# Kernel optimization log

Hardware: AMD Instinct MI355X
Metric: run time of the kernel (lower is better)

The kernel has to match this reference:

```python
import jax, jax.numpy as jnp
import numpy as np

N_NODES = 100000


def gcn_conv(x, W, b, src, dst, n):
    """PyG GCNConv with default add_self_loops and symmetric normalization."""
    xw = x @ W  # [N, out]
    loop = jnp.arange(n, dtype=src.dtype)
    s = jnp.concatenate([src, loop])  # source j
    d = jnp.concatenate([dst, loop])  # target i
    deg = jax.ops.segment_sum(jnp.ones_like(d, dtype=xw.dtype), d, num_segments=n)
    dinv = jnp.where(deg > 0, jax.lax.rsqrt(deg), 0.0)
    norm = dinv[s] * dinv[d]  # [E+N]
    msg = xw[s] * norm[:, None]
    out = jax.ops.segment_sum(msg, d, num_segments=n)
    return out + b


def setup_inputs() -> dict:
    key = jax.random.key(0)
    ks = jax.random.split(key, 9)
    n, e, f = N_NODES, 1600000, 512
    x = jax.random.normal(ks[0], (n, f), dtype=jnp.float32)
    edge_index = jax.random.randint(ks[1], (2, e), 0, n, dtype=jnp.int32)
    y = jax.random.uniform(ks[2], (n, 1), dtype=jnp.float32)
    W1 = jax.random.normal(ks[3], (f, 64), dtype=jnp.float32) / np.sqrt(f)
    b1 = jnp.zeros((64,), jnp.float32)
    W2 = jax.random.normal(ks[4], (64, 256), dtype=jnp.float32) / np.sqrt(64)
    b2 = jnp.zeros((256,), jnp.float32)
    W3 = jax.random.normal(ks[5], (256, 1), dtype=jnp.float32) / np.sqrt(256)
    b3 = jnp.zeros((1,), jnp.float32)
    return {"x": x, "edge_index": edge_index, "y": y,
            "W1": W1, "b1": b1, "W2": W2, "b2": b2, "W3": W3, "b3": b3}


def reference(x, edge_index, y, W1, b1, W2, b2, W3, b3):
    n = x.shape[0]
    src, dst = edge_index[0], edge_index[1]
    h = jax.nn.relu(gcn_conv(x, W1, b1, src, dst, n))
    # dropout is identity in eval mode
    h = jax.nn.relu(gcn_conv(h, W2, b2, src, dst, n))
    z = gcn_conv(h, W3, b3, src, dst, n)  # logits [N, 1]
    # BCE(sigmoid(z), y), computed stably via log-sigmoid
    loss = -(y * jax.nn.log_sigmoid(z) + (1.0 - y) * jax.nn.log_sigmoid(-z))
    return jnp.mean(loss)
```

## Files before the change

kernel.cpp:

```cpp
#include <hip/hip_runtime.h>
#include <math.h>

typedef __attribute__((ext_vector_type(8))) short s16x8;
typedef __attribute__((ext_vector_type(4))) float f32x4;

__device__ inline ushort f2bf(float f) {
    union { float f; unsigned u; } v; v.f = f;
    unsigned r = v.u + 0x7FFF + ((v.u >> 16) & 1);
    return (ushort)(r >> 16);
}
__device__ inline float bf2f(ushort h) {
    union { unsigned u; float f; } v; v.u = ((unsigned)h) << 16;
    return v.f;
}
__device__ inline float bfLo(unsigned u) {
    union { unsigned x; float f; } v; v.x = u << 16; return v.f;
}
__device__ inline float bfHi(unsigned u) {
    union { unsigned x; float f; } v; v.x = u & 0xFFFF0000u; return v.f;
}


__global__ void hist_kernel(const int* __restrict__ dst, int E, int* __restrict__ cnt) {
    int e = blockIdx.x * blockDim.x + threadIdx.x;
    if (e < E) atomicAdd(&cnt[dst[e]], 1);
}

__global__ void alloc_kernel(const int* __restrict__ cnt, int* __restrict__ row_start,
                             float* __restrict__ dinv, int* __restrict__ total, int N) {
    int i = blockIdx.x * blockDim.x + threadIdx.x;
    int lane = threadIdx.x & 63;
    int c = (i < N) ? cnt[i] : 0;
    int inc = c;
#pragma unroll
    for (int o = 1; o < 64; o <<= 1) {
        int v = __shfl_up(inc, o, 64);
        if (lane >= o) inc += v;
    }
    int wsum = __shfl(inc, 63, 64);
    int base = 0;
    if (lane == 0) base = atomicAdd(total, wsum);
    base = __shfl(base, 0, 64);
    if (i < N) {
        row_start[i] = base + inc - c;
        dinv[i] = rsqrtf((float)(c + 1));
    }
}

__global__ void scatter_kernel(const int* __restrict__ src, const int* __restrict__ dst, int E,
                               const int* __restrict__ row_start, int* __restrict__ cursor,
                               int* __restrict__ csr) {
    int e = blockIdx.x * blockDim.x + threadIdx.x;
    if (e < E) {
        int d = dst[e];
        int p = row_start[d] + atomicAdd(&cursor[d], 1);
        csr[p] = src[e];
    }
}

__global__ void wsplit_kernel(const float* __restrict__ W, ushort* __restrict__ wt_hi,
                              ushort* __restrict__ wt_lo) {
    int idx = blockIdx.x * blockDim.x + threadIdx.x;
    if (idx < 64 * 512) {
        int n = idx & 63, k = idx >> 6;
        float f = W[k * 64 + n];
        ushort h = f2bf(f);
        wt_hi[n * 512 + k] = h;
        wt_lo[n * 512 + k] = f2bf(f - bf2f(h));
    }
}

__global__ __launch_bounds__(256, 3) void gemm1_kernel(const float* __restrict__ x,
                                                       const ushort* __restrict__ wt_hi,
                                                       const ushort* __restrict__ wt_lo,
                                                       const float* __restrict__ dinv,
                                                       ushort* __restrict__ out, int N) {
    __shared__ __align__(16) short xs_hi[128 * 64];
    __shared__ __align__(16) short xs_lo[128 * 64];
    __shared__ __align__(16) short ws_hi[64 * 64];
    __shared__ __align__(16) short ws_lo[64 * 64];

    const int tid = threadIdx.x;
    const int nodeBase = blockIdx.x * 128;
    const int wave = tid >> 6, lane = tid & 63;
    const int m16 = lane & 15, quad = lane >> 4;

    f32x4 acc[2][4];
#pragma unroll
    for (int mt = 0; mt < 2; mt++)
#pragma unroll
        for (int nt = 0; nt < 4; nt++) acc[mt][nt] = (f32x4){0.f, 0.f, 0.f, 0.f};

    for (int kc = 0; kc < 512; kc += 64) {
        __syncthreads();
#pragma unroll
        for (int i = 0; i < 4; i++) {
            int f = tid + i * 256;
            int node = f >> 3, g = f & 7;
            int gn = nodeBase + node;
            if (gn >= N) gn = N - 1;
            const float4 a = *(const float4*)(x + (size_t)gn * 512 + kc + g * 8);
            const float4 b = *(const float4*)(x + (size_t)gn * 512 + kc + g * 8 + 4);
            float ff[8] = {a.x, a.y, a.z, a.w, b.x, b.y, b.z, b.w};
            union { ushort u[8]; uint4 v; } H, L;
#pragma unroll
            for (int j = 0; j < 8; j++) {
                ushort h = f2bf(ff[j]);
                H.u[j] = h;
                L.u[j] = f2bf(ff[j] - bf2f(h));
            }
            int gp = (g + node) & 7;
            *(uint4*)&xs_hi[node * 64 + gp * 8] = H.v;
            *(uint4*)&xs_lo[node * 64 + gp * 8] = L.v;
        }
#pragma unroll
        for (int i = 0; i < 2; i++) {
            int f = tid + i * 256;
            int n = f >> 3, g = f & 7;
            int gp = (g + n) & 7;
            *(uint4*)&ws_hi[n * 64 + gp * 8] =
                *(const uint4*)(wt_hi + (size_t)n * 512 + kc + g * 8);
            *(uint4*)&ws_lo[n * 64 + gp * 8] =
                *(const uint4*)(wt_lo + (size_t)n * 512 + kc + g * 8);
        }
        __syncthreads();
#pragma unroll
        for (int ck = 0; ck < 2; ck++) {
            s16x8 Ah[2], Al[2];
#pragma unroll
            for (int mt = 0; mt < 2; mt++) {
                int row = (wave * 2 + mt) * 16 + m16;
                int gp = (ck * 4 + quad + row) & 7;
                Ah[mt] = *(s16x8*)&xs_hi[row * 64 + gp * 8];
                Al[mt] = *(s16x8*)&xs_lo[row * 64 + gp * 8];
            }
#pragma unroll
            for (int nt = 0; nt < 4; nt++) {
                int n = nt * 16 + m16;
                int gp = (ck * 4 + quad + n) & 7;
                s16x8 Bh = *(s16x8*)&ws_hi[n * 64 + gp * 8];
                s16x8 Bl = *(s16x8*)&ws_lo[n * 64 + gp * 8];
#pragma unroll
                for (int mt = 0; mt < 2; mt++) {
                    acc[mt][nt] = __builtin_amdgcn_mfma_f32_16x16x32_bf16(Ah[mt], Bh, acc[mt][nt], 0, 0, 0);
                    acc[mt][nt] = __builtin_amdgcn_mfma_f32_16x16x32_bf16(Ah[mt], Bl, acc[mt][nt], 0, 0, 0);
                    acc[mt][nt] = __builtin_amdgcn_mfma_f32_16x16x32_bf16(Al[mt], Bh, acc[mt][nt], 0, 0, 0);
                }
            }
        }
    }
#pragma unroll
    for (int mt = 0; mt < 2; mt++) {
#pragma unroll
        for (int r = 0; r < 4; r++) {
            int gn = nodeBase + (wave * 2 + mt) * 16 + quad * 4 + r;
            if (gn < N) {
                float di = dinv[gn];
#pragma unroll
                for (int nt = 0; nt < 4; nt++)
                    out[(size_t)gn * 64 + nt * 16 + m16] = f2bf(di * acc[mt][nt][r]);
            }
        }
    }
}

template <int RELU, int BIAS, int PREMUL>
__global__ void agg64bf_kernel(const ushort* __restrict__ in, ushort* __restrict__ out,
                               const int* __restrict__ row_start, const int* __restrict__ cnt,
                               const int* __restrict__ csr, const float* __restrict__ dinv,
                               const float* __restrict__ bias, int N) {
    int gw = (int)((blockIdx.x * (size_t)blockDim.x + threadIdx.x) >> 6);
    int lane = threadIdx.x & 63;
    if (gw >= N) return;
    float acc = bf2f(in[(size_t)gw * 64 + lane]);
    int s = row_start[gw];
    int c = cnt[gw];
    int e = 0;
    for (; e + 8 <= c; e += 8) {
        int j0 = csr[s + e + 0], j1 = csr[s + e + 1], j2 = csr[s + e + 2], j3 = csr[s + e + 3];
        int j4 = csr[s + e + 4], j5 = csr[s + e + 5], j6 = csr[s + e + 6], j7 = csr[s + e + 7];
        float v0 = bf2f(in[(size_t)j0 * 64 + lane]);
        float v1 = bf2f(in[(size_t)j1 * 64 + lane]);
        float v2 = bf2f(in[(size_t)j2 * 64 + lane]);
        float v3 = bf2f(in[(size_t)j3 * 64 + lane]);
        float v4 = bf2f(in[(size_t)j4 * 64 + lane]);
        float v5 = bf2f(in[(size_t)j5 * 64 + lane]);
        float v6 = bf2f(in[(size_t)j6 * 64 + lane]);
        float v7 = bf2f(in[(size_t)j7 * 64 + lane]);
        acc += ((v0 + v1) + (v2 + v3)) + ((v4 + v5) + (v6 + v7));
    }
    for (; e < c; e++) {
        int j = csr[s + e];
        acc += bf2f(in[(size_t)j * 64 + lane]);
    }
    float di = dinv[gw];
    float v = di * acc;
    if (BIAS) v += bias[lane];
    if (RELU) v = fmaxf(v, 0.f);
    if (PREMUL) v *= di;
    out[(size_t)gw * 64 + lane] = f2bf(v);
}

__global__ __launch_bounds__(256, 2) void gemm23_kernel(const ushort* __restrict__ a2,
                                                        const float* __restrict__ W2,
                                                        const float* __restrict__ b2,
                                                        const float* __restrict__ W3,
                                                        const float* __restrict__ dinv,
                                                        float* __restrict__ r, int N) {
    __shared__ float w2s[64 * 256];
    __shared__ float b2s[256];
    __shared__ float w3s[256];
    const int tid = threadIdx.x;
#pragma unroll
    for (int i = 0; i < 16; i++) {
        int f4 = tid + i * 256;
        *(float4*)&w2s[f4 * 4] = *(const float4*)&W2[f4 * 4];
    }
    b2s[tid] = b2[tid];
    w3s[tid] = W3[tid];
    __syncthreads();

    const int lane = tid & 63;
    const int wave = tid >> 6;
    const int nodeBase = blockIdx.x * 64 + wave * 16;

    float4 w3f = *(const float4*)&w3s[lane * 4];
    float4 b2f = *(const float4*)&b2s[lane * 4];

    float acc[16][4];
#pragma unroll
    for (int n = 0; n < 16; n++) {
        acc[n][0] = 0.f; acc[n][1] = 0.f; acc[n][2] = 0.f; acc[n][3] = 0.f;
    }

    for (int k4 = 0; k4 < 64; k4 += 4) {
        float4 wf0 = *(const float4*)&w2s[(k4 + 0) * 256 + lane * 4];
        float4 wf1 = *(const float4*)&w2s[(k4 + 1) * 256 + lane * 4];
        float4 wf2 = *(const float4*)&w2s[(k4 + 2) * 256 + lane * 4];
        float4 wf3 = *(const float4*)&w2s[(k4 + 3) * 256 + lane * 4];
#pragma unroll
        for (int n = 0; n < 16; n++) {
            int gn = nodeBase + n;
            if (gn >= N) gn = N - 1;
            uint2 u = *(const uint2*)(a2 + (size_t)gn * 64 + k4);
            float a0 = bfLo(u.x), a1 = bfHi(u.x), a2v = bfLo(u.y), a3 = bfHi(u.y);
            acc[n][0] = fmaf(a0, wf0.x, acc[n][0]);
            acc[n][1] = fmaf(a0, wf0.y, acc[n][1]);
            acc[n][2] = fmaf(a0, wf0.z, acc[n][2]);
            acc[n][3] = fmaf(a0, wf0.w, acc[n][3]);
            acc[n][0] = fmaf(a1, wf1.x, acc[n][0]);
            acc[n][1] = fmaf(a1, wf1.y, acc[n][1]);
            acc[n][2] = fmaf(a1, wf1.z, acc[n][2]);
            acc[n][3] = fmaf(a1, wf1.w, acc[n][3]);
            acc[n][0] = fmaf(a2v, wf2.x, acc[n][0]);
            acc[n][1] = fmaf(a2v, wf2.y, acc[n][1]);
            acc[n][2] = fmaf(a2v, wf2.z, acc[n][2]);
            acc[n][3] = fmaf(a2v, wf2.w, acc[n][3]);
            acc[n][0] = fmaf(a3, wf3.x, acc[n][0]);
            acc[n][1] = fmaf(a3, wf3.y, acc[n][1]);
            acc[n][2] = fmaf(a3, wf3.z, acc[n][2]);
            acc[n][3] = fmaf(a3, wf3.w, acc[n][3]);
        }
    }

#pragma unroll
    for (int n = 0; n < 16; n++) {
        float r0 = fmaxf(acc[n][0] + b2f.x, 0.f);
        float r1 = fmaxf(acc[n][1] + b2f.y, 0.f);
        float r2 = fmaxf(acc[n][2] + b2f.z, 0.f);
        float r3 = fmaxf(acc[n][3] + b2f.w, 0.f);
        float p = r0 * w3f.x + r1 * w3f.y + r2 * w3f.z + r3 * w3f.w;
#pragma unroll
        for (int off = 32; off > 0; off >>= 1) p += __shfl_down(p, off, 64);
        int gn = nodeBase + n;
        if (lane == 0 && gn < N) r[gn] = dinv[gn] * p;
    }
}

__global__ void loss_kernel(const float* __restrict__ r, const float* __restrict__ dinv,
                            const int* __restrict__ row_start, const int* __restrict__ cnt,
                            const int* __restrict__ csr, const float* __restrict__ y,
                            const float* __restrict__ b3, float* __restrict__ out,
                            int N, float invN) {
    int i = blockIdx.x * blockDim.x + threadIdx.x;
    float loss = 0.f;
    if (i < N) {
        float aedge = r[i];
        int s = row_start[i], c = cnt[i];
        int e = 0;
        for (; e + 4 <= c; e += 4) {
            int j0 = csr[s + e + 0], j1 = csr[s + e + 1];
            int j2 = csr[s + e + 2], j3 = csr[s + e + 3];
            aedge += (r[j0] + r[j1]) + (r[j2] + r[j3]);
        }
        for (; e < c; e++) aedge += r[csr[s + e]];
        float z = dinv[i] * aedge + b3[0];
        float yv = y[i];
        float L = log1pf(expf(-fabsf(z)));
        float spz  = fmaxf(z, 0.f) + L;
        float spnz = fmaxf(-z, 0.f) + L;
        loss = yv * spnz + (1.f - yv) * spz;
    }
#pragma unroll
    for (int off = 32; off > 0; off >>= 1) loss += __shfl_down(loss, off, 64);
    __shared__ float red[4];
    int lane = threadIdx.x & 63, wave = threadIdx.x >> 6;
    if (lane == 0) red[wave] = loss;
    __syncthreads();
    if (threadIdx.x == 0)
        atomicAdd(out, (red[0] + red[1] + red[2] + red[3]) * invN);
}

extern "C" void kernel_launch(void* const* d_in, const int* in_sizes, int n_in,
                              void* d_out, int out_size, void* d_ws, size_t ws_size,
                              hipStream_t stream) {
    const float* x  = (const float*)d_in[0];
    const int*   ei = (const int*)d_in[1];
    const float* y  = (const float*)d_in[2];
    const float* W1 = (const float*)d_in[3];
    const float* b1 = (const float*)d_in[4];
    const float* W2 = (const float*)d_in[5];
    const float* b2 = (const float*)d_in[6];
    const float* W3 = (const float*)d_in[7];
    const float* b3 = (const float*)d_in[8];

    const int N = in_sizes[2];
    const int E = in_sizes[1] / 2;
    const int* src  = ei;
    const int* dstp = ei + E;

    char* w = (char*)d_ws;
    int*    cnt       = (int*)w;    w += (size_t)N * 4;
    int*    cursor    = (int*)w;    w += (size_t)N * 4;
    int*    total     = (int*)w;    w += 16;
    int*    row_start = (int*)w;    w += (size_t)N * 4;
    float*  dinv      = (float*)w;  w += (size_t)N * 4;
    int*    csr       = (int*)w;    w += (size_t)E * 4;
    ushort* wt_hi     = (ushort*)w; w += (size_t)64 * 512 * 2;
    ushort* wt_lo     = (ushort*)w; w += (size_t)64 * 512 * 2;
    ushort* pbuf      = (ushort*)w; w += (size_t)N * 64 * 2;
    ushort* qbuf      = (ushort*)w; w += (size_t)N * 64 * 2;
    float*  rbuf      = (float*)w;  w += (size_t)N * 4;

    hipMemsetAsync(cnt, 0, (size_t)N * 8 + 16, stream);
    hipMemsetAsync(d_out, 0, sizeof(float), stream);

    const int tb = 256;
    wsplit_kernel<<<(64 * 512 + tb - 1) / tb, tb, 0, stream>>>(W1, wt_hi, wt_lo);
    hist_kernel<<<(E + tb - 1) / tb, tb, 0, stream>>>(dstp, E, cnt);
    alloc_kernel<<<(N + tb - 1) / tb, tb, 0, stream>>>(cnt, row_start, dinv, total, N);
    scatter_kernel<<<(E + tb - 1) / tb, tb, 0, stream>>>(src, dstp, E, row_start, cursor, csr);

    gemm1_kernel<<<(N + 127) / 128, 256, 0, stream>>>(x, wt_hi, wt_lo, dinv, pbuf, N);
    agg64bf_kernel<1, 1, 1><<<(N + 3) / 4, 256, 0, stream>>>(pbuf, qbuf, row_start, cnt, csr, dinv, b1, N);
    agg64bf_kernel<0, 0, 0><<<(N + 3) / 4, 256, 0, stream>>>(qbuf, pbuf, row_start, cnt, csr, dinv, nullptr, N);

    gemm23_kernel<<<(N + 63) / 64, 256, 0, stream>>>(pbuf, W2, b2, W3, dinv, rbuf, N);

    loss_kernel<<<(N + tb - 1) / tb, tb, 0, stream>>>(rbuf, dinv, row_start, cnt, csr, y, b3,
                                                      (float*)d_out, N, 1.0f / N);
}
```

Baseline: 732.1 us.

## Split aggregation across edges per wave with 16-byte gathers and wave-per-node loss

The 64-wide bf16 aggregation kernel now splits each wave into eight edge groups of eight lanes. Each lane gathers a 16-byte chunk (8 bf16 features) from one neighbour, and the partial sums are combined with shuffles, which replaces one 2-byte load per lane per edge and raises memory-level parallelism. The loss kernel changes from one thread per node to one wave per node, so neighbour reads are spread across lanes instead of run as a serial loop. The risks are idle lanes on low-degree nodes (average degree about 16), extra shuffle reductions, and launching 64x more threads for the loss.

```diff
diff --git a/kernel.cpp b/kernel.cpp
--- a/kernel.cpp
+++ b/kernel.cpp
@@ -18,6 +18,9 @@
 }
 __device__ inline float bfHi(unsigned u) {
     union { unsigned x; float f; } v; v.x = u & 0xFFFF0000u; return v.f;
+}
+__device__ inline unsigned pk(float a, float b) {
+    return (unsigned)f2bf(a) | ((unsigned)f2bf(b) << 16);
 }
 
 
@@ -170,35 +173,51 @@
                                const int* __restrict__ csr, const float* __restrict__ dinv,
                                const float* __restrict__ bias, int N) {
     int gw = (int)((blockIdx.x * (size_t)blockDim.x + threadIdx.x) >> 6);
-    int lane = threadIdx.x & 63;
     if (gw >= N) return;
-    float acc = bf2f(in[(size_t)gw * 64 + lane]);
-    int s = row_start[gw];
-    int c = cnt[gw];
-    int e = 0;
-    for (; e + 8 <= c; e += 8) {
-        int j0 = csr[s + e + 0], j1 = csr[s + e + 1], j2 = csr[s + e + 2], j3 = csr[s + e + 3];
-        int j4 = csr[s + e + 4], j5 = csr[s + e + 5], j6 = csr[s + e + 6], j7 = csr[s + e + 7];
-        float v0 = bf2f(in[(size_t)j0 * 64 + lane]);
-        float v1 = bf2f(in[(size_t)j1 * 64 + lane]);
-        float v2 = bf2f(in[(size_t)j2 * 64 + lane]);
-        float v3 = bf2f(in[(size_t)j3 * 64 + lane]);
-        float v4 = bf2f(in[(size_t)j4 * 64 + lane]);
-        float v5 = bf2f(in[(size_t)j5 * 64 + lane]);
-        float v6 = bf2f(in[(size_t)j6 * 64 + lane]);
-        float v7 = bf2f(in[(size_t)j7 * 64 + lane]);
-        acc += ((v0 + v1) + (v2 + v3)) + ((v4 + v5) + (v6 + v7));
-    }
-    for (; e < c; e++) {
-        int j = csr[s + e];
-        acc += bf2f(in[(size_t)j * 64 + lane]);
-    }
-    float di = dinv[gw];
-    float v = di * acc;
-    if (BIAS) v += bias[lane];
-    if (RELU) v = fmaxf(v, 0.f);
-    if (PREMUL) v *= di;
-    out[(size_t)gw * 64 + lane] = f2bf(v);
+    const int lane = threadIdx.x & 63;
+    const int f8 = lane & 7, e8 = lane >> 3;
+    const int s = row_start[gw], c = cnt[gw];
+
+    float acc[8];
+#pragma unroll
+    for (int k = 0; k < 8; k++) acc[k] = 0.f;
+
+    for (int base = 0; base < c; base += 8) {
+        int e = base + e8;
+        int ec = (e < c) ? e : (c - 1);
+        int j = csr[s + ec];
+        uint4 u = *(const uint4*)(in + (size_t)j * 64 + f8 * 8);
+        float valid = (e < c) ? 1.f : 0.f;
+        acc[0] += valid * bfLo(u.x); acc[1] += valid * bfHi(u.x);
+        acc[2] += valid * bfLo(u.y); acc[3] += valid * bfHi(u.y);
+        acc[4] += valid * bfLo(u.z); acc[5] += valid * bfHi(u.z);
+        acc[6] += valid * bfLo(u.w); acc[7] += valid * bfHi(u.w);
+    }
+#pragma unroll
+    for (int off = 32; off >= 8; off >>= 1) {
+#pragma unroll
+        for (int k = 0; k < 8; k++) acc[k] += __shfl_down(acc[k], off, 64);
+    }
+    if (e8 == 0) {
+        uint4 su = *(const uint4*)(in + (size_t)gw * 64 + f8 * 8);
+        acc[0] += bfLo(su.x); acc[1] += bfHi(su.x);
+        acc[2] += bfLo(su.y); acc[3] += bfHi(su.y);
+        acc[4] += bfLo(su.z); acc[5] += bfHi(su.z);
+        acc[6] += bfLo(su.w); acc[7] += bfHi(su.w);
+        float di = dinv[gw];
+#pragma unroll
+        for (int k = 0; k < 8; k++) {
+            float v = di * acc[k];
+            if (BIAS) v += bias[f8 * 8 + k];
+            if (RELU) v = fmaxf(v, 0.f);
+            if (PREMUL) v *= di;
+            acc[k] = v;
+        }
+        uint4 o;
+        o.x = pk(acc[0], acc[1]); o.y = pk(acc[2], acc[3]);
+        o.z = pk(acc[4], acc[5]); o.w = pk(acc[6], acc[7]);
+        *(uint4*)(out + (size_t)gw * 64 + f8 * 8) = o;
+    }
 }
 
 __global__ __launch_bounds__(256, 2) void gemm23_kernel(const ushort* __restrict__ a2,
@@ -282,29 +301,28 @@
                             const int* __restrict__ csr, const float* __restrict__ y,
                             const float* __restrict__ b3, float* __restrict__ out,
                             int N, float invN) {
-    int i = blockIdx.x * blockDim.x + threadIdx.x;
+    const int lane = threadIdx.x & 63, wave = threadIdx.x >> 6;
+    int gw = (int)((blockIdx.x * (size_t)blockDim.x + threadIdx.x) >> 6);
     float loss = 0.f;
-    if (i < N) {
-        float aedge = r[i];
-        int s = row_start[i], c = cnt[i];
-        int e = 0;
-        for (; e + 4 <= c; e += 4) {
-            int j0 = csr[s + e + 0], j1 = csr[s + e + 1];
-            int j2 = csr[s + e + 2], j3 = csr[s + e + 3];
-            aedge += (r[j0] + r[j1]) + (r[j2] + r[j3]);
-        }
-        for (; e < c; e++) aedge += r[csr[s + e]];
-        float z = dinv[i] * aedge + b3[0];
-        float yv = y[i];
-        float L = log1pf(expf(-fabsf(z)));
-        float spz  = fmaxf(z, 0.f) + L;
-        float spnz = fmaxf(-z, 0.f) + L;
-        loss = yv * spnz + (1.f - yv) * spz;
-    }
-#pragma unroll
-    for (int off = 32; off > 0; off >>= 1) loss += __shfl_down(loss, off, 64);
+    if (gw < N) {
+        int s = row_start[gw], c = cnt[gw];
+        float sum = 0.f;
+        for (int base = 0; base < c; base += 64) {
+            int e = base + lane;
+            if (e < c) sum += r[csr[s + e]];
+        }
+#pragma unroll
+        for (int off = 32; off > 0; off >>= 1) sum += __shfl_down(sum, off, 64);
+        if (lane == 0) {
+            float z = dinv[gw] * (sum + r[gw]) + b3[0];
+            float yv = y[gw];
+            float L = log1pf(expf(-fabsf(z)));
+            float spz  = fmaxf(z, 0.f) + L;
+            float spnz = fmaxf(-z, 0.f) + L;
+            loss = yv * spnz + (1.f - yv) * spz;
+        }
+    }
     __shared__ float red[4];
-    int lane = threadIdx.x & 63, wave = threadIdx.x >> 6;
     if (lane == 0) red[wave] = loss;
     __syncthreads();
     if (threadIdx.x == 0)
@@ -357,6 +375,6 @@
 
     gemm23_kernel<<<(N + 63) / 64, 256, 0, stream>>>(pbuf, W2, b2, W3, dinv, rbuf, N);
 
-    loss_kernel<<<(N + tb - 1) / tb, tb, 0, stream>>>(rbuf, dinv, row_start, cnt, csr, y, b3,
-                                                      (float*)d_out, N, 1.0f / N);
-}
+    loss_kernel<<<(N + 3) / 4, 256, 0, stream>>>(rbuf, dinv, row_start, cnt, csr, y, b3,
+                                                 (float*)d_out, N, 1.0f / N);
+}
```

New measurement: 1.007 ms. 37.6% more time.
